# Performance work log

Hardware: AMD Instinct MI355X
Metric: run time of the kernel (lower is better)

## Reference

```python
import jax, jax.numpy as jnp
import numpy as np

INPUT_SIZE = 34
HIDDEN = 4
NUM_CLASSES = 3
B, T = 4096, 200


def setup_inputs() -> dict:
    key = jax.random.key(0)
    ks = jax.random.split(key, 8)
    k = 1.0 / np.sqrt(HIDDEN)  # torch default uniform init bound
    u = lambda kk, shape: jax.random.uniform(kk, shape, jnp.float32, -k, k)
    x = jax.random.normal(ks[0], (B, T, INPUT_SIZE), jnp.float32)
    W_ih = u(ks[1], (4 * HIDDEN, INPUT_SIZE))   # gate order: i, f, g, o
    W_hh = u(ks[2], (4 * HIDDEN, HIDDEN))
    b_ih = u(ks[3], (4 * HIDDEN,))
    b_hh = u(ks[4], (4 * HIDDEN,))
    W_fc = u(ks[5], (NUM_CLASSES, HIDDEN))
    b_fc = u(ks[6], (NUM_CLASSES,))
    return {"x": x, "W_ih": W_ih, "W_hh": W_hh, "b_ih": b_ih,
            "b_hh": b_hh, "W_fc": W_fc, "b_fc": b_fc}


def reference(x, W_ih, W_hh, b_ih, b_hh, W_fc, b_fc):
    Bsz = x.shape[0]
    H = W_hh.shape[1]
    # Precompute input contributions for all timesteps: [B, T, 4H]
    x_gates = jnp.einsum('btd,gd->btg', x, W_ih) + b_ih + b_hh
    x_gates = jnp.swapaxes(x_gates, 0, 1)  # [T, B, 4H] for scan

    def step(carry, xg_t):
        h, c = carry
        gates = xg_t + h @ W_hh.T          # [B, 4H]
        i, f, g, o = jnp.split(gates, 4, axis=-1)
        i = jax.nn.sigmoid(i)
        f = jax.nn.sigmoid(f)
        g = jnp.tanh(g)
        o = jax.nn.sigmoid(o)
        c = f * c + i * g
        h = o * jnp.tanh(c)
        return (h, c), None

    h0 = jnp.zeros((Bsz, H), x.dtype)
    c0 = jnp.zeros((Bsz, H), x.dtype)
    (h_last, _), _ = jax.lax.scan(step, (h0, c0), x_gates)
    # dropout is identity in eval mode
    return h_last @ W_fc.T + b_fc  # [B, num_classes]
```

## Files before the change

kernel.cpp:

```cpp
#include <hip/hip_runtime.h>

#define B_SZ 4096
#define T_SZ 200
#define IN_SZ 34

__device__ __forceinline__ float sigf(float x) {
    return 1.0f / (1.0f + __expf(-x));
}
__device__ __forceinline__ float tanh_f(float x) {
    return 2.0f / (1.0f + __expf(-2.0f * x)) - 1.0f;
}

__device__ __forceinline__ float quad_bcast0(float v) {
    int s = __float_as_int(v);
    return __int_as_float(__builtin_amdgcn_update_dpp(s, s, 0x00, 0xf, 0xf, true));
}
__device__ __forceinline__ float quad_bcast1(float v) {
    int s = __float_as_int(v);
    return __int_as_float(__builtin_amdgcn_update_dpp(s, s, 0x55, 0xf, 0xf, true));
}
__device__ __forceinline__ float quad_bcast2(float v) {
    int s = __float_as_int(v);
    return __int_as_float(__builtin_amdgcn_update_dpp(s, s, 0xAA, 0xf, 0xf, true));
}
__device__ __forceinline__ float quad_bcast3(float v) {
    int s = __float_as_int(v);
    return __int_as_float(__builtin_amdgcn_update_dpp(s, s, 0xFF, 0xf, 0xf, true));
}

typedef const __attribute__((address_space(1))) unsigned int* gas_t;
typedef __attribute__((address_space(3))) unsigned int* las_t;

__global__ __launch_bounds__(64) void xgates_kernel(
    const float* __restrict__ x, const float* __restrict__ W_ih,
    const float* __restrict__ b_ih, const float* __restrict__ b_hh,
    float* __restrict__ xg) {
  __shared__ float xs[64 * IN_SZ];
  int lane = threadIdx.x;
  const float4* src = reinterpret_cast<const float4*>(x + (size_t)blockIdx.x * 64 * IN_SZ);
  char* ldsb = reinterpret_cast<char*>(xs);
  #pragma unroll
  for (int i = 0; i < 8; ++i) {
    __builtin_amdgcn_global_load_lds((gas_t)(src + i * 64 + lane),
                                     (las_t)(ldsb + i * 1024), 16, 0, 0);
  }
  if (lane < 32) {
    __builtin_amdgcn_global_load_lds((gas_t)(src + 512 + lane),
                                     (las_t)(ldsb + 8192), 16, 0, 0);
  }
  __syncthreads();

  float xr[IN_SZ];
  const float2* rp = reinterpret_cast<const float2*>(&xs[lane * IN_SZ]);
  #pragma unroll
  for (int k = 0; k < IN_SZ / 2; ++k) {
    float2 v = rp[k];
    xr[2 * k] = v.x;
    xr[2 * k + 1] = v.y;
  }
  float acc[16];
  #pragma unroll
  for (int g = 0; g < 16; ++g) acc[g] = b_ih[g] + b_hh[g];
  #pragma unroll
  for (int k = 0; k < IN_SZ; ++k) {
    #pragma unroll
    for (int g = 0; g < 16; ++g)
      acc[g] = fmaf(xr[k], W_ih[g * IN_SZ + k], acc[g]);
  }
  size_t row = (size_t)blockIdx.x * 64 + lane;
  float4* op = reinterpret_cast<float4*>(xg + row * 16);
  #pragma unroll
  for (int j = 0; j < 4; ++j)
    op[j] = make_float4(acc[j], acc[4 + j], acc[8 + j], acc[12 + j]);
}

#define U_SZ 10
__global__ __launch_bounds__(64) void lstm_scan(
    const float* __restrict__ xg, const float* __restrict__ W_hh,
    const float* __restrict__ W_fc, const float* __restrict__ b_fc,
    float* __restrict__ out) {
  int tid = blockIdx.x * 64 + threadIdx.x;
  int b = tid >> 2;
  int j = tid & 3;
  float Wi[4], Wf[4], Wg[4], Wo[4];
  #pragma unroll
  for (int k = 0; k < 4; ++k) {
    Wi[k] = W_hh[(0 + j) * 4 + k];
    Wf[k] = W_hh[(4 + j) * 4 + k];
    Wg[k] = W_hh[(8 + j) * 4 + k];
    Wo[k] = W_hh[(12 + j) * 4 + k];
  }
  float h[4] = {0.f, 0.f, 0.f, 0.f};
  float c = 0.f;

  auto step = [&](float4 g4) {
    float pi = g4.x, pf = g4.y, pg = g4.z, po = g4.w;
    #pragma unroll
    for (int k = 0; k < 4; ++k) {
      pi = fmaf(Wi[k], h[k], pi);
      pf = fmaf(Wf[k], h[k], pf);
      pg = fmaf(Wg[k], h[k], pg);
      po = fmaf(Wo[k], h[k], po);
    }
    float iv = sigf(pi);
    float fv = sigf(pf);
    float gv = tanh_f(pg);
    float ov = sigf(po);
    c = fmaf(fv, c, iv * gv);
    float hj = ov * tanh_f(c);
    h[0] = quad_bcast0(hj);
    h[1] = quad_bcast1(hj);
    h[2] = quad_bcast2(hj);
    h[3] = quad_bcast3(hj);
  };

  const float4* xp = reinterpret_cast<const float4*>(xg) + (size_t)b * (T_SZ * 4) + j;
  float4 bufA[U_SZ], bufB[U_SZ];
  #pragma unroll
  for (int u = 0; u < U_SZ; ++u) bufA[u] = xp[4 * u];

  #pragma unroll 1
  for (int blk = 0; blk < 20; blk += 2) {
    const float4* p1 = xp + (size_t)(blk + 1) * (4 * U_SZ);
    #pragma unroll
    for (int u = 0; u < U_SZ; ++u) bufB[u] = p1[4 * u];
    #pragma unroll
    for (int u = 0; u < U_SZ; ++u) step(bufA[u]);
    if (blk + 2 < 20) {
      const float4* p2 = xp + (size_t)(blk + 2) * (4 * U_SZ);
      #pragma unroll
      for (int u = 0; u < U_SZ; ++u) bufA[u] = p2[4 * u];
    }
    #pragma unroll
    for (int u = 0; u < U_SZ; ++u) step(bufB[u]);
  }

  if (j < 3) {
    float acc = b_fc[j];
    #pragma unroll
    for (int k = 0; k < 4; ++k) acc = fmaf(W_fc[j * 4 + k], h[k], acc);
    out[b * 3 + j] = acc;
  }
}

__global__ __launch_bounds__(256) void lstm_fused(
    const float* __restrict__ x, const float* __restrict__ W_ih,
    const float* __restrict__ W_hh, const float* __restrict__ b_ih,
    const float* __restrict__ b_hh, const float* __restrict__ W_fc,
    const float* __restrict__ b_fc, float* __restrict__ out) {
  __shared__ float Ws[16 * IN_SZ];
  for (int i = threadIdx.x; i < 16 * IN_SZ; i += 256) Ws[i] = W_ih[i];
  __syncthreads();
  int tid = blockIdx.x * 256 + threadIdx.x;
  int b = tid >> 2;
  int j = tid & 3;
  float bi = b_ih[0 + j] + b_hh[0 + j];
  float bf = b_ih[4 + j] + b_hh[4 + j];
  float bg = b_ih[8 + j] + b_hh[8 + j];
  float bo = b_ih[12 + j] + b_hh[12 + j];
  float Wi[4], Wf[4], Wg[4], Wo[4];
  #pragma unroll
  for (int k = 0; k < 4; ++k) {
    Wi[k] = W_hh[(0 + j) * 4 + k];
    Wf[k] = W_hh[(4 + j) * 4 + k];
    Wg[k] = W_hh[(8 + j) * 4 + k];
    Wo[k] = W_hh[(12 + j) * 4 + k];
  }
  float h[4] = {0.f, 0.f, 0.f, 0.f};
  float c = 0.f;
  const float2* xp = reinterpret_cast<const float2*>(x + (size_t)b * T_SZ * IN_SZ);
  int lbase = (threadIdx.x & 63) & ~3;
  for (int t = 0; t < T_SZ; ++t) {
    float xr[IN_SZ];
    #pragma unroll
    for (int k = 0; k < IN_SZ / 2; ++k) {
      float2 v = xp[(size_t)t * (IN_SZ / 2) + k];
      xr[2 * k] = v.x;
      xr[2 * k + 1] = v.y;
    }
    float pi = bi, pf = bf, pg = bg, po = bo;
    #pragma unroll
    for (int k = 0; k < IN_SZ; ++k) {
      pi = fmaf(xr[k], Ws[(0 + j) * IN_SZ + k], pi);
      pf = fmaf(xr[k], Ws[(4 + j) * IN_SZ + k], pf);
      pg = fmaf(xr[k], Ws[(8 + j) * IN_SZ + k], pg);
      po = fmaf(xr[k], Ws[(12 + j) * IN_SZ + k], po);
    }
    #pragma unroll
    for (int k = 0; k < 4; ++k) {
      pi = fmaf(Wi[k], h[k], pi);
      pf = fmaf(Wf[k], h[k], pf);
      pg = fmaf(Wg[k], h[k], pg);
      po = fmaf(Wo[k], h[k], po);
    }
    float iv = sigf(pi);
    float fv = sigf(pf);
    float gv = tanh_f(pg);
    float ov = sigf(po);
    c = fmaf(fv, c, iv * gv);
    float hj = ov * tanh_f(c);
    h[0] = __shfl(hj, lbase + 0);
    h[1] = __shfl(hj, lbase + 1);
    h[2] = __shfl(hj, lbase + 2);
    h[3] = __shfl(hj, lbase + 3);
  }
  if (j < 3) {
    float acc = b_fc[j];
    #pragma unroll
    for (int k = 0; k < 4; ++k) acc = fmaf(W_fc[j * 4 + k], h[k], acc);
    out[b * 3 + j] = acc;
  }
}

extern "C" void kernel_launch(void* const* d_in, const int* in_sizes, int n_in,
                              void* d_out, int out_size, void* d_ws, size_t ws_size,
                              hipStream_t stream) {
  const float* x    = (const float*)d_in[0];
  const float* W_ih = (const float*)d_in[1];
  const float* W_hh = (const float*)d_in[2];
  const float* b_ih = (const float*)d_in[3];
  const float* b_hh = (const float*)d_in[4];
  const float* W_fc = (const float*)d_in[5];
  const float* b_fc = (const float*)d_in[6];
  float* out = (float*)d_out;

  const size_t need = (size_t)B_SZ * T_SZ * 16 * sizeof(float);
  if (ws_size >= need) {
    float* xg = (float*)d_ws;
    hipLaunchKernelGGL(xgates_kernel, dim3(B_SZ * T_SZ / 64), dim3(64), 0, stream,
                       x, W_ih, b_ih, b_hh, xg);
    hipLaunchKernelGGL(lstm_scan, dim3(B_SZ * 4 / 64), dim3(64), 0, stream,
                       xg, W_hh, W_fc, b_fc, out);
  } else {
    hipLaunchKernelGGL(lstm_fused, dim3(B_SZ * 4 / 256), dim3(256), 0, stream,
                       x, W_ih, W_hh, b_ih, b_hh, W_fc, b_fc, out);
  }
}
```

Before: 85.63 us.

## Store precomputed gate inputs in fp16 and make xgates kernel persistent with double-buffered LDS

The intermediate x-gate buffer is now written and read as half precision, halving the workspace traffic between the projection kernel and the scan kernel. The projection kernel becomes a persistent grid of 1024 two-wave blocks that loop over tiles, prefetching the next tile into a second LDS buffer via global_load_lds while computing the current one. This trades numerical precision of the gate pre-activations (fp16 rounding before the 200-step recurrence) for reduced memory bandwidth and fewer block launches.

After: 86.94 us. No clear change (+1.5%).

```diff
diff --git a/kernel.cpp b/kernel.cpp
--- a/kernel.cpp
+++ b/kernel.cpp
@@ -1,8 +1,12 @@
 #include <hip/hip_runtime.h>
+#include <hip/hip_fp16.h>
 
 #define B_SZ 4096
 #define T_SZ 200
 #define IN_SZ 34
+#define TILES (B_SZ * T_SZ / 64)
+#define XG_BLOCKS 1024
+#define WAVES_TOTAL (XG_BLOCKS * 2)
 
 __device__ __forceinline__ float sigf(float x) {
     return 1.0f / (1.0f + __expf(-x));
@@ -31,52 +35,85 @@
 typedef const __attribute__((address_space(1))) unsigned int* gas_t;
 typedef __attribute__((address_space(3))) unsigned int* las_t;
 
-__global__ __launch_bounds__(64) void xgates_kernel(
+__global__ __launch_bounds__(128) void xgates_kernel(
     const float* __restrict__ x, const float* __restrict__ W_ih,
     const float* __restrict__ b_ih, const float* __restrict__ b_hh,
-    float* __restrict__ xg) {
-  __shared__ float xs[64 * IN_SZ];
-  int lane = threadIdx.x;
-  const float4* src = reinterpret_cast<const float4*>(x + (size_t)blockIdx.x * 64 * IN_SZ);
-  char* ldsb = reinterpret_cast<char*>(xs);
-  #pragma unroll
-  for (int i = 0; i < 8; ++i) {
-    __builtin_amdgcn_global_load_lds((gas_t)(src + i * 64 + lane),
-                                     (las_t)(ldsb + i * 1024), 16, 0, 0);
-  }
-  if (lane < 32) {
-    __builtin_amdgcn_global_load_lds((gas_t)(src + 512 + lane),
-                                     (las_t)(ldsb + 8192), 16, 0, 0);
-  }
-  __syncthreads();
-
-  float xr[IN_SZ];
-  const float2* rp = reinterpret_cast<const float2*>(&xs[lane * IN_SZ]);
-  #pragma unroll
-  for (int k = 0; k < IN_SZ / 2; ++k) {
-    float2 v = rp[k];
-    xr[2 * k] = v.x;
-    xr[2 * k + 1] = v.y;
-  }
-  float acc[16];
-  #pragma unroll
-  for (int g = 0; g < 16; ++g) acc[g] = b_ih[g] + b_hh[g];
-  #pragma unroll
-  for (int k = 0; k < IN_SZ; ++k) {
-    #pragma unroll
-    for (int g = 0; g < 16; ++g)
-      acc[g] = fmaf(xr[k], W_ih[g * IN_SZ + k], acc[g]);
-  }
-  size_t row = (size_t)blockIdx.x * 64 + lane;
-  float4* op = reinterpret_cast<float4*>(xg + row * 16);
-  #pragma unroll
-  for (int j = 0; j < 4; ++j)
-    op[j] = make_float4(acc[j], acc[4 + j], acc[8 + j], acc[12 + j]);
+    __half* __restrict__ xg) {
+  __shared__ float xs[2 * 2 * 64 * IN_SZ];
+  const int lane = threadIdx.x & 63;
+  const int wv = threadIdx.x >> 6;
+  float* buf0 = &xs[wv * 2 * 64 * IN_SZ];
+  float* buf1 = buf0 + 64 * IN_SZ;
+  const int gw = blockIdx.x * 2 + wv;
+
+  float bias[16];
+  #pragma unroll
+  for (int g = 0; g < 16; ++g) bias[g] = b_ih[g] + b_hh[g];
+
+  auto issue = [&](int tile, float* buf) {
+    const float4* src = reinterpret_cast<const float4*>(x + (size_t)tile * 64 * IN_SZ);
+    char* l = reinterpret_cast<char*>(buf);
+    #pragma unroll
+    for (int i = 0; i < 8; ++i)
+      __builtin_amdgcn_global_load_lds((gas_t)(src + i * 64 + lane),
+                                       (las_t)(l + i * 1024), 16, 0, 0);
+    if (lane < 32)
+      __builtin_amdgcn_global_load_lds((gas_t)(src + 512 + lane),
+                                       (las_t)(l + 8192), 16, 0, 0);
+  };
+
+  int tile = gw;
+  if (tile < TILES) issue(tile, buf0);
+  int cur = 0;
+  #pragma unroll 1
+  for (; tile < TILES; tile += WAVES_TOTAL) {
+    int nxt = tile + WAVES_TOTAL;
+    if (nxt < TILES) {
+      issue(nxt, cur ? buf0 : buf1);
+      asm volatile("s_waitcnt vmcnt(9)" ::: "memory");
+    } else {
+      asm volatile("s_waitcnt vmcnt(0)" ::: "memory");
+    }
+    __builtin_amdgcn_sched_barrier(0);
+
+    const float* buf = cur ? buf1 : buf0;
+    float xr[IN_SZ];
+    const float2* rp = reinterpret_cast<const float2*>(buf + lane * IN_SZ);
+    #pragma unroll
+    for (int k = 0; k < IN_SZ / 2; ++k) {
+      float2 v = rp[k];
+      xr[2 * k] = v.x;
+      xr[2 * k + 1] = v.y;
+    }
+    float acc[16];
+    #pragma unroll
+    for (int g = 0; g < 16; ++g) acc[g] = bias[g];
+    #pragma unroll
+    for (int k = 0; k < IN_SZ; ++k) {
+      #pragma unroll
+      for (int g = 0; g < 16; ++g)
+        acc[g] = fmaf(xr[k], W_ih[g * IN_SZ + k], acc[g]);
+    }
+    union {
+      __half2 h[8];
+      int4 v[2];
+    } u;
+    #pragma unroll
+    for (int j = 0; j < 4; ++j) {
+      u.h[2 * j + 0] = __floats2half2_rn(acc[0 + j], acc[4 + j]);
+      u.h[2 * j + 1] = __floats2half2_rn(acc[8 + j], acc[12 + j]);
+    }
+    size_t row = (size_t)tile * 64 + lane;
+    int4* op = reinterpret_cast<int4*>(xg + row * 16);
+    op[0] = u.v[0];
+    op[1] = u.v[1];
+    cur ^= 1;
+  }
 }
 
 #define U_SZ 10
 __global__ __launch_bounds__(64) void lstm_scan(
-    const float* __restrict__ xg, const float* __restrict__ W_hh,
+    const __half* __restrict__ xg, const float* __restrict__ W_hh,
     const float* __restrict__ W_fc, const float* __restrict__ b_fc,
     float* __restrict__ out) {
   int tid = blockIdx.x * 64 + threadIdx.x;
@@ -93,8 +130,15 @@
   float h[4] = {0.f, 0.f, 0.f, 0.f};
   float c = 0.f;
 
-  auto step = [&](float4 g4) {
-    float pi = g4.x, pf = g4.y, pg = g4.z, po = g4.w;
+  auto step = [&](uint2 w) {
+    union {
+      uint2 u;
+      __half2 h2[2];
+    } v;
+    v.u = w;
+    float2 p01 = __half22float2(v.h2[0]);
+    float2 p23 = __half22float2(v.h2[1]);
+    float pi = p01.x, pf = p01.y, pg = p23.x, po = p23.y;
     #pragma unroll
     for (int k = 0; k < 4; ++k) {
       pi = fmaf(Wi[k], h[k], pi);
@@ -114,20 +158,20 @@
     h[3] = quad_bcast3(hj);
   };
 
-  const float4* xp = reinterpret_cast<const float4*>(xg) + (size_t)b * (T_SZ * 4) + j;
-  float4 bufA[U_SZ], bufB[U_SZ];
+  const uint2* xp = reinterpret_cast<const uint2*>(xg) + (size_t)b * (T_SZ * 4) + j;
+  uint2 bufA[U_SZ], bufB[U_SZ];
   #pragma unroll
   for (int u = 0; u < U_SZ; ++u) bufA[u] = xp[4 * u];
 
   #pragma unroll 1
   for (int blk = 0; blk < 20; blk += 2) {
-    const float4* p1 = xp + (size_t)(blk + 1) * (4 * U_SZ);
+    const uint2* p1 = xp + (size_t)(blk + 1) * (4 * U_SZ);
     #pragma unroll
     for (int u = 0; u < U_SZ; ++u) bufB[u] = p1[4 * u];
     #pragma unroll
     for (int u = 0; u < U_SZ; ++u) step(bufA[u]);
     if (blk + 2 < 20) {
-      const float4* p2 = xp + (size_t)(blk + 2) * (4 * U_SZ);
+      const uint2* p2 = xp + (size_t)(blk + 2) * (4 * U_SZ);
       #pragma unroll
       for (int u = 0; u < U_SZ; ++u) bufA[u] = p2[4 * u];
     }
@@ -224,10 +268,10 @@
   const float* b_fc = (const float*)d_in[6];
   float* out = (float*)d_out;
 
-  const size_t need = (size_t)B_SZ * T_SZ * 16 * sizeof(float);
+  const size_t need = (size_t)B_SZ * T_SZ * 16 * sizeof(__half);
   if (ws_size >= need) {
-    float* xg = (float*)d_ws;
-    hipLaunchKernelGGL(xgates_kernel, dim3(B_SZ * T_SZ / 64), dim3(64), 0, stream,
+    __half* xg = (__half*)d_ws;
+    hipLaunchKernelGGL(xgates_kernel, dim3(XG_BLOCKS), dim3(128), 0, stream,
                        x, W_ih, b_ih, b_hh, xg);
     hipLaunchKernelGGL(lstm_scan, dim3(B_SZ * 4 / 64), dim3(64), 0, stream,
                        xg, W_hh, W_fc, b_fc, out);
```
